# Kernel optimization log

Hardware: AMD Instinct MI355X
Metric: run time of the kernel (lower is better)

## Reference

```python
import jax, jax.numpy as jnp
import numpy as np

N_NODES = 100000
N_EDGES = 1600000
HIDDEN = 128
LEAKY_SLOPE = 0.01  # torch F.leaky_relu default


def setup_inputs() -> dict:
    key = jax.random.key(0)
    k1, k2, k3, k4 = jax.random.split(key, 4)
    x = jax.random.normal(k1, (N_NODES, HIDDEN), dtype=jnp.float32)
    edge_index = jax.random.randint(k2, (2, N_EDGES), 0, N_NODES, dtype=jnp.int64)
    # nn.Linear(hidden, 1, bias=False) weights, stored as [hidden] vectors
    w_i = jax.random.normal(k3, (HIDDEN,), dtype=jnp.float32) * (1.0 / np.sqrt(HIDDEN))
    w_j = jax.random.normal(k4, (HIDDEN,), dtype=jnp.float32) * (1.0 / np.sqrt(HIDDEN))
    return {"x": x, "edge_index": edge_index, "w_i": w_i, "w_j": w_j}


def _segment_softmax(e, seg, num_segments):
    # numerically stable softmax over variable-length groups keyed by seg
    seg_max = jax.ops.segment_max(e, seg, num_segments=num_segments)
    seg_max = jnp.where(jnp.isfinite(seg_max), seg_max, 0.0)  # empty segments
    e_exp = jnp.exp(e - seg_max[seg])
    denom = jax.ops.segment_sum(e_exp, seg, num_segments=num_segments)
    return e_exp / denom[seg]


def reference(x, edge_index, w_i, w_j):
    n = x.shape[0]
    idx_j = edge_index[0]  # edge_index_j (softmax groups)
    idx_i = edge_index[1]  # edge_index_i (aggregation destinations)
    # per-node attention logits, gathered per edge
    ei_all = x @ w_i  # [N]
    ej_all = x @ w_j  # [N]
    e = ei_all[idx_i] + ej_all[idx_j]  # [E]
    e = jnp.where(e > 0, e, LEAKY_SLOPE * e)  # leaky_relu
    alpha = _segment_softmax(e.astype(jnp.float32), idx_j, n)  # [E]
    # spmm(edge_index[[1,0]], alpha, N, N, x): out[idx_i] += alpha * x[idx_j]
    msgs = alpha[:, None] * x[idx_j]  # [E, hidden]
    out = jax.ops.segment_sum(msgs, idx_i, num_segments=n)
    return jax.nn.relu(out)
```

## Files before the change

### kernel.cpp

```cpp
#include <hip/hip_runtime.h>

#define N_HID 128
#define LEAKY 0.01f
#define EPB   2048
#define SCB   1024
#define TABV(g) (tab[g] + bs1[(g) >> 10])

__device__ inline int load_idx(const void* eidx, long long pos, int is64) {
    if (is64) return (int)((const long long*)eidx)[pos];
    return ((const int*)eidx)[pos];
}

__device__ inline int detect64(const void* eidx, int lane) {
    const long long* p = (const long long*)eidx;
    unsigned long long b = __ballot((p[lane] >> 32) != 0);
    return b == 0ull;
}

__global__ __launch_bounds__(256) void logits_hist_k(
        const float* __restrict__ x, const float* __restrict__ w_i,
        const float* __restrict__ w_j, float* __restrict__ ei_all,
        float* __restrict__ ej_all, signed char* __restrict__ xq,
        float* __restrict__ xs, const void* __restrict__ eidx,
        unsigned* __restrict__ tabI, unsigned* __restrict__ tabJ,
        int n, long long E, int nblkA, int NB) {
    __shared__ unsigned hi[512], hj[512];
    int lane = threadIdx.x & 63;
    if (blockIdx.x < (unsigned)nblkA) {
        for (int b = threadIdx.x; b < NB; b += 256) { hi[b] = 0; hj[b] = 0; }
        __syncthreads();
        int is64 = detect64(eidx, lane);
        long long k0 = (long long)blockIdx.x * EPB;
        #pragma unroll 4
        for (int m = 0; m < EPB / 256; ++m) {
            long long k = k0 + m * 256 + threadIdx.x;
            if (k < E) {
                int j = load_idx(eidx, k, is64);
                int i = load_idx(eidx, E + k, is64);
                atomicAdd(&hi[i >> 8], 1u);
                atomicAdd(&hj[j >> 8], 1u);
            }
        }
        __syncthreads();
        for (int b = threadIdx.x; b < NB; b += 256) {
            tabI[(size_t)b * nblkA + blockIdx.x] = hi[b];
            tabJ[(size_t)b * nblkA + blockIdx.x] = hj[b];
        }
    } else {
        int blk = blockIdx.x - nblkA;
        int wave = blk * 4 + (int)(threadIdx.x >> 6);
        if (wave >= n) return;
        const float2* xr = (const float2*)(x + (long long)wave * N_HID);
        float2 v  = xr[lane];
        float2 wi = ((const float2*)w_i)[lane];
        float2 wj = ((const float2*)w_j)[lane];
        float si = v.x * wi.x + v.y * wi.y;
        float sj = v.x * wj.x + v.y * wj.y;
        float am = fmaxf(fabsf(v.x), fabsf(v.y));
        #pragma unroll
        for (int off = 32; off >= 1; off >>= 1) {
            si += __shfl_xor(si, off);
            sj += __shfl_xor(sj, off);
            am = fmaxf(am, __shfl_xor(am, off));
        }
        if (xq) {
            float inv = 127.f / fmaxf(am, 1e-20f);
            int q0 = (int)rintf(v.x * inv);
            int q1 = (int)rintf(v.y * inv);
            q0 = min(127, max(-127, q0));
            q1 = min(127, max(-127, q1));
            ushort pk = (ushort)((q0 & 0xff) | ((q1 & 0xff) << 8));
            ((ushort*)(xq + (size_t)wave * N_HID))[lane] = pk;
        }
        if (lane == 0) {
            ei_all[wave] = si;
            ej_all[wave] = sj;
            if (xq) xs[wave] = fmaxf(am, 1e-20f) * (1.f / 127.f);
        }
    }
}

__global__ __launch_bounds__(SCB) void scanT1_k(unsigned* __restrict__ a,
                                                unsigned* __restrict__ bs, int nt) {
    __shared__ unsigned tmp[SCB];
    int gid = blockIdx.x * SCB + threadIdx.x;
    unsigned v = (gid < nt) ? a[gid] : 0;
    tmp[threadIdx.x] = v;
    __syncthreads();
    for (int off = 1; off < SCB; off <<= 1) {
        unsigned t = (threadIdx.x >= off) ? tmp[threadIdx.x - off] : 0;
        __syncthreads();
        tmp[threadIdx.x] += t;
        __syncthreads();
    }
    if (gid < nt) a[gid] = tmp[threadIdx.x] - v;
    if (threadIdx.x == SCB - 1) bs[blockIdx.x] = tmp[threadIdx.x];
}

__global__ __launch_bounds__(SCB) void scanT2_k(unsigned* __restrict__ bs, int nb) {
    __shared__ unsigned tmp[SCB];
    unsigned v = (threadIdx.x < nb) ? bs[threadIdx.x] : 0;
    tmp[threadIdx.x] = v;
    __syncthreads();
    for (int off = 1; off < SCB; off <<= 1) {
        unsigned t = (threadIdx.x >= off) ? tmp[threadIdx.x - off] : 0;
        __syncthreads();
        tmp[threadIdx.x] += t;
        __syncthreads();
    }
    if (threadIdx.x < nb) bs[threadIdx.x] = tmp[threadIdx.x] - v;
}

__global__ __launch_bounds__(256) void scatter2_k(
        const void* __restrict__ eidx, const unsigned* __restrict__ tab,
        const unsigned* __restrict__ bs1, unsigned* __restrict__ srecI,
        unsigned* __restrict__ srecJ, long long E, int nblkA, int NB, int NT) {
    __shared__ unsigned ci[512], cj[512];
    unsigned Eu = (unsigned)E;
    for (int b = threadIdx.x; b < NB; b += 256) {
        size_t gI = (size_t)b * nblkA + blockIdx.x;
        size_t gJ = (size_t)NT + gI;
        ci[b] = TABV(gI);
        cj[b] = TABV(gJ) - Eu;
    }
    __syncthreads();
    int is64 = detect64(eidx, threadIdx.x & 63);
    long long k0 = (long long)blockIdx.x * EPB;
    #pragma unroll 4
    for (int m = 0; m < EPB / 256; ++m) {
        long long k = k0 + m * 256 + threadIdx.x;
        if (k < E) {
            int j = load_idx(eidx, k, is64);
            int i = load_idx(eidx, E + k, is64);
            unsigned pI = atomicAdd(&ci[i >> 8], 1u);
            srecI[pI] = ((unsigned)(i & 255) << 17) | (unsigned)j;
            unsigned pJ = atomicAdd(&cj[j >> 8], 1u);
            srecJ[pJ] = ((unsigned)(j & 255) << 17) | (unsigned)i;
        }
    }
}

__global__ __launch_bounds__(512) void finalizeJ_k(
        const unsigned* __restrict__ srecJ, const unsigned* __restrict__ tab,
        const unsigned* __restrict__ bs1, const float* __restrict__ ei_all,
        const float* __restrict__ ej_all, float2* __restrict__ ejd,
        int n, long long E, int nblkA, int NB, int NT) {
    int b = blockIdx.x;
    int tid = threadIdx.x;
    unsigned Eu = (unsigned)E;
    size_t gJ0 = (size_t)NT + (size_t)b * nblkA;
    int base = (int)(TABV(gJ0) - Eu);
    int end  = (b + 1 < NB) ? (int)(TABV(gJ0 + nblkA) - Eu) : (int)E;

    __shared__ float ejl[256];
    __shared__ float dsum[256];
    int g = b * 256 + tid;
    if (tid < 256) {
        ejl[tid]  = (g < n) ? ej_all[g] : 0.f;
        dsum[tid] = 0.f;
    }
    __syncthreads();

    for (int t = base + tid; t < end; t += 512) {
        unsigned r = srecJ[t];
        int jl = (int)(r >> 17);
        int i  = (int)(r & 0x1FFFFu);
        float e = ei_all[i] + ejl[jl];
        e = e > 0.f ? e : LEAKY * e;
        atomicAdd(&dsum[jl], __expf(e));
    }
    __syncthreads();
    if (tid < 256 && g < n) {
        float2 r2;
        r2.x = ejl[tid];
        r2.y = dsum[tid];
        ejd[g] = r2;
    }
}

__global__ __launch_bounds__(512) void finalizeI_k(
        const unsigned* __restrict__ srecI, const unsigned* __restrict__ tab,
        const unsigned* __restrict__ bs1, const float* __restrict__ ei_all,
        const float2* __restrict__ ejd, int* __restrict__ start,
        unsigned* __restrict__ pje, int n, long long E, int nblkA, int NB,
        int NT) {
    int b = blockIdx.x;
    int tid = threadIdx.x;
    size_t gI0 = (size_t)b * nblkA;
    int base = (int)TABV(gI0);
    int end  = (b + 1 < NB) ? (int)TABV(gI0 + nblkA) : (int)E;

    __shared__ int cnt[256];
    __shared__ int off[256];
    __shared__ float eil[256];
    int g = b * 256 + tid;
    if (tid < 256) {
        cnt[tid] = 0;
        eil[tid] = (g < n) ? ei_all[g] : 0.f;
    }
    __syncthreads();

    for (int t = base + tid; t < end; t += 512)
        atomicAdd(&cnt[srecI[t] >> 17], 1);
    __syncthreads();

    int v = 0;
    if (tid < 256) { v = cnt[tid]; off[tid] = v; }
    __syncthreads();
    for (int s = 1; s < 256; s <<= 1) {
        int t2 = 0;
        if (tid < 256 && tid >= s) t2 = off[tid - s];
        __syncthreads();
        if (tid < 256) off[tid] += t2;
        __syncthreads();
    }
    if (tid < 256) {
        int excl = off[tid] - v;
        if (g < n) start[g] = base + excl;
        cnt[tid] = excl;
    }
    if (b == NB - 1 && tid == 0) start[n] = (int)E;
    __syncthreads();

    for (int t = base + tid; t < end; t += 512) {
        unsigned r = srecI[t];
        int il = (int)(r >> 17);
        int j  = (int)(r & 0x1FFFFu);
        float2 ed = ejd[j];
        float e = eil[il] + ed.x;
        e = e > 0.f ? e : LEAKY * e;
        float alpha = __expf(e) / ed.y;
        unsigned aq = __float2uint_rn(alpha * 32768.f);
        if (aq > 32767u) aq = 32767u;
        int slot = base + atomicAdd(&cnt[il], 1);
        pje[slot] = ((unsigned)j << 15) | aq;
    }
}

#define ACC4(w, A, B, C, D, af)                      \
    A += af * (float)((int)((w) << 24) >> 24);       \
    B += af * (float)((int)((w) << 16) >> 24);       \
    C += af * (float)((int)((w) <<  8) >> 24);       \
    D += af * (float)((int)(w) >> 24);

__global__ __launch_bounds__(256) void gather_i8_k(
        const int* __restrict__ start, const unsigned* __restrict__ pje,
        const signed char* __restrict__ xq, const float* __restrict__ xs,
        float* __restrict__ out, int n) {
    int wave = (int)((blockIdx.x * (long long)blockDim.x + threadIdx.x) >> 6);
    int lane = threadIdx.x & 63;
    if (wave >= n) return;
    int s = start[wave];
    int e_end = start[wave + 1];
    int sub = lane >> 3;
    int col = lane & 7;

    float t0 = 0.f, t1 = 0.f, t2 = 0.f, t3 = 0.f;
    float t4 = 0.f, t5 = 0.f, t6 = 0.f, t7 = 0.f;
    float t8 = 0.f, t9 = 0.f, tA = 0.f, tB = 0.f;
    float tC = 0.f, tD = 0.f, tE = 0.f, tF = 0.f;
    for (int e = s; e < e_end; e += 16) {
        int ee0 = e + sub;
        int ee1 = e + 8 + sub;
        unsigned c0 = (ee0 < e_end) ? pje[ee0] : 0u;
        unsigned c1 = (ee1 < e_end) ? pje[ee1] : 0u;
        int j0 = (int)(c0 >> 15), j1 = (int)(c1 >> 15);
        float a0 = (float)(c0 & 0x7FFFu) * (1.f / 32768.f) * xs[j0];
        float a1 = (float)(c1 & 0x7FFFu) * (1.f / 32768.f) * xs[j1];
        uint4 u0 = ((const uint4*)(xq + (size_t)j0 * N_HID))[col];
        uint4 u1 = ((const uint4*)(xq + (size_t)j1 * N_HID))[col];
        ACC4(u0.x, t0, t1, t2, t3, a0)
        ACC4(u0.y, t4, t5, t6, t7, a0)
        ACC4(u0.z, t8, t9, tA, tB, a0)
        ACC4(u0.w, tC, tD, tE, tF, a0)
        ACC4(u1.x, t0, t1, t2, t3, a1)
        ACC4(u1.y, t4, t5, t6, t7, a1)
        ACC4(u1.z, t8, t9, tA, tB, a1)
        ACC4(u1.w, tC, tD, tE, tF, a1)
    }
    #pragma unroll
    for (int off = 8; off <= 32; off <<= 1) {
        t0 += __shfl_xor(t0, off); t1 += __shfl_xor(t1, off);
        t2 += __shfl_xor(t2, off); t3 += __shfl_xor(t3, off);
        t4 += __shfl_xor(t4, off); t5 += __shfl_xor(t5, off);
        t6 += __shfl_xor(t6, off); t7 += __shfl_xor(t7, off);
        t8 += __shfl_xor(t8, off); t9 += __shfl_xor(t9, off);
        tA += __shfl_xor(tA, off); tB += __shfl_xor(tB, off);
        tC += __shfl_xor(tC, off); tD += __shfl_xor(tD, off);
        tE += __shfl_xor(tE, off); tF += __shfl_xor(tF, off);
    }
    if (sub == 0) {
        float4* orow = (float4*)(out + (size_t)wave * N_HID);
        float4 r;
        r.x = fmaxf(t0, 0.f); r.y = fmaxf(t1, 0.f);
        r.z = fmaxf(t2, 0.f); r.w = fmaxf(t3, 0.f);
        orow[col * 4 + 0] = r;
        r.x = fmaxf(t4, 0.f); r.y = fmaxf(t5, 0.f);
        r.z = fmaxf(t6, 0.f); r.w = fmaxf(t7, 0.f);
        orow[col * 4 + 1] = r;
        r.x = fmaxf(t8, 0.f); r.y = fmaxf(t9, 0.f);
        r.z = fmaxf(tA, 0.f); r.w = fmaxf(tB, 0.f);
        orow[col * 4 + 2] = r;
        r.x = fmaxf(tC, 0.f); r.y = fmaxf(tD, 0.f);
        r.z = fmaxf(tE, 0.f); r.w = fmaxf(tF, 0.f);
        orow[col * 4 + 3] = r;
    }
}

__global__ __launch_bounds__(256) void gather_f32_k(
        const int* __restrict__ start, const unsigned* __restrict__ pje,
        const float* __restrict__ x, float* __restrict__ out, int n) {
    int wave = (int)((blockIdx.x * (long long)blockDim.x + threadIdx.x) >> 6);
    int lane = threadIdx.x & 63;
    if (wave >= n) return;
    int s = start[wave];
    int e_end = start[wave + 1];
    float ax = 0.f, ay = 0.f;
    unsigned ja = 0;
    if (s < e_end) ja = pje[s];
    for (int e = s; e < e_end; ++e) {
        unsigned cur = ja;
        if (e + 1 < e_end) ja = pje[e + 1];
        float a = (float)(cur & 0x7FFFu) * (1.f / 32768.f);
        float2 v = ((const float2*)(x + (long long)(cur >> 15) * N_HID))[lane];
        ax += a * v.x;
        ay += a * v.y;
    }
    float2 r;
    r.x = fmaxf(ax, 0.f);
    r.y = fmaxf(ay, 0.f);
    ((float2*)(out + (long long)wave * N_HID))[lane] = r;
}

extern "C" void kernel_launch(void* const* d_in, const int* in_sizes, int n_in,
                              void* d_out, int out_size, void* d_ws,
                              size_t ws_size, hipStream_t stream) {
    const float* x   = (const float*)d_in[0];
    const void*  eix = d_in[1];
    const float* w_i = (const float*)d_in[2];
    const float* w_j = (const float*)d_in[3];
    float* out = (float*)d_out;

    int n = in_sizes[0] / N_HID;
    long long E = in_sizes[1] / 2;

    int nblkA = (int)((E + EPB - 1) / EPB);
    int nblkL = (n + 3) / 4;
    int NB    = (n + 255) / 256;
    int NT    = NB * nblkA;
    int NT2   = 2 * NT;
    int nb1   = (NT2 + SCB - 1) / SCB;

    char* p = (char*)d_ws;
    float* ei_all = (float*)p;               p += (size_t)n * 4;
    float* ej_all = (float*)p;               p += (size_t)n * 4;
    float2* ejd   = (float2*)p;              p += (size_t)n * 8;
    int*   start  = (int*)p;                 p += ((size_t)(n + 1) * 4 + 15) & ~15ull;
    unsigned* tab = (unsigned*)p;            p += ((size_t)NT2 * 4 + 15) & ~15ull;
    unsigned* tabI = tab;
    unsigned* tabJ = tab + NT;
    unsigned* bs1 = (unsigned*)p;            p += (size_t)SCB * 4;
    unsigned* srecI = (unsigned*)p;          p += (size_t)E * 4;
    unsigned* pje   = (unsigned*)p;          p += (size_t)E * 4;
    unsigned* srecJ = pje;
    signed char* xq = (signed char*)p;       p += ((size_t)n * N_HID + 15) & ~15ull;
    float* xs     = (float*)p;               p += (size_t)n * 4;
    int wsBig = ((size_t)(p - (char*)d_ws) <= ws_size);
    if (!wsBig) { xq = nullptr; xs = nullptr; }

    logits_hist_k<<<(unsigned)(nblkA + nblkL), 256, 0, stream>>>(
        x, w_i, w_j, ei_all, ej_all, xq, xs, eix, tabI, tabJ, n, E, nblkA, NB);

    scanT1_k<<<nb1, SCB, 0, stream>>>(tab, bs1, NT2);
    scanT2_k<<<1, SCB, 0, stream>>>(bs1, nb1);

    scatter2_k<<<nblkA, 256, 0, stream>>>(eix, tab, bs1, srecI, srecJ,
                                          E, nblkA, NB, NT);

    finalizeJ_k<<<NB, 512, 0, stream>>>(srecJ, tab, bs1, ei_all, ej_all, ejd,
                                        n, E, nblkA, NB, NT);

    finalizeI_k<<<NB, 512, 0, stream>>>(srecI, tab, bs1, ei_all, ejd,
                                        start, pje, n, E, nblkA, NB, NT);

    long long t4 = (long long)n * 64;
    if (wsBig) {
        gather_i8_k<<<(unsigned)((t4 + 255) / 256), 256, 0, stream>>>(
            start, pje, xq, xs, out, n);
    } else {
        gather_f32_k<<<(unsigned)((t4 + 255) / 256), 256, 0, stream>>>(
            start, pje, x, out, n);
    }
}
```

Baseline: 169.0 us.

## Fuse finalizeI and int8 gather into one block kernel with LDS edge list

Merges the per-destination alpha computation and the int8 gather-aggregate into one kernel. Each 1024-thread block buckets its 256 destination nodes' edges in shared memory (falling back to global when the block has more than CAP edges) and then aggregates them directly. This drops a kernel launch, the global pje write and read round trip, and the start array. finalizeJ is also moved to 1024 threads. The trade-off is fewer blocks (NB, about 391), each with 16 waves handling 16 nodes serially, which may lower gather parallelism and latency hiding.

```diff
diff --git a/kernel.cpp b/kernel.cpp
--- a/kernel.cpp
+++ b/kernel.cpp
@@ -4,6 +4,7 @@
 #define LEAKY 0.01f
 #define EPB   2048
 #define SCB   1024
+#define CAP   5120
 #define TABV(g) (tab[g] + bs1[(g) >> 10])
 
 __device__ inline int load_idx(const void* eidx, long long pos, int is64) {
@@ -140,7 +141,7 @@
     }
 }
 
-__global__ __launch_bounds__(512) void finalizeJ_k(
+__global__ __launch_bounds__(1024) void finalizeJ_k(
         const unsigned* __restrict__ srecJ, const unsigned* __restrict__ tab,
         const unsigned* __restrict__ bs1, const float* __restrict__ ei_all,
         const float* __restrict__ ej_all, float2* __restrict__ ejd,
@@ -161,7 +162,7 @@
     }
     __syncthreads();
 
-    for (int t = base + tid; t < end; t += 512) {
+    for (int t = base + tid; t < end; t += 1024) {
         unsigned r = srecJ[t];
         int jl = (int)(r >> 17);
         int i  = (int)(r & 0x1FFFFu);
@@ -175,6 +176,145 @@
         r2.x = ejl[tid];
         r2.y = dsum[tid];
         ejd[g] = r2;
+    }
+}
+
+#define ACC4(w, A, B, C, D, af)                      \
+    A += af * (float)((int)((w) << 24) >> 24);       \
+    B += af * (float)((int)((w) << 16) >> 24);       \
+    C += af * (float)((int)((w) <<  8) >> 24);       \
+    D += af * (float)((int)(w) >> 24);
+
+__global__ __launch_bounds__(1024) void finalizeI_gather_k(
+        const unsigned* __restrict__ srecI, const unsigned* __restrict__ tab,
+        const unsigned* __restrict__ bs1, const float* __restrict__ ei_all,
+        const float2* __restrict__ ejd, const signed char* __restrict__ xq,
+        const float* __restrict__ xs, unsigned* __restrict__ pjeG,
+        float* __restrict__ out, int n, long long E, int nblkA, int NB,
+        int NT) {
+    int b = blockIdx.x;
+    int tid = threadIdx.x;
+    size_t gI0 = (size_t)b * nblkA;
+    int base = (int)TABV(gI0);
+    int end  = (b + 1 < NB) ? (int)TABV(gI0 + nblkA) : (int)E;
+    bool useLds = (end - base) <= CAP;
+
+    __shared__ int cnt[256];
+    __shared__ int off[256];
+    __shared__ int lstart[256];
+    __shared__ float eil[256];
+    __shared__ unsigned pjeL[CAP];
+    int g = b * 256 + tid;
+    if (tid < 256) {
+        cnt[tid] = 0;
+        eil[tid] = (g < n) ? ei_all[g] : 0.f;
+    }
+    __syncthreads();
+
+    for (int t = base + tid; t < end; t += 1024)
+        atomicAdd(&cnt[srecI[t] >> 17], 1);
+    __syncthreads();
+
+    int v = 0;
+    if (tid < 256) { v = cnt[tid]; off[tid] = v; }
+    __syncthreads();
+    for (int s = 1; s < 256; s <<= 1) {
+        int t2 = 0;
+        if (tid < 256 && tid >= s) t2 = off[tid - s];
+        __syncthreads();
+        if (tid < 256) off[tid] += t2;
+        __syncthreads();
+    }
+    if (tid < 256) {
+        int excl = off[tid] - v;
+        lstart[tid] = excl;
+        cnt[tid] = excl;
+    }
+    __syncthreads();
+
+    for (int t = base + tid; t < end; t += 1024) {
+        unsigned r = srecI[t];
+        int il = (int)(r >> 17);
+        int j  = (int)(r & 0x1FFFFu);
+        float2 ed = ejd[j];
+        float e = eil[il] + ed.x;
+        e = e > 0.f ? e : LEAKY * e;
+        float alpha = __expf(e) / ed.y;
+        unsigned aq = __float2uint_rn(alpha * 32768.f);
+        if (aq > 32767u) aq = 32767u;
+        int slot = atomicAdd(&cnt[il], 1);
+        unsigned rec = ((unsigned)j << 15) | aq;
+        if (useLds) pjeL[slot] = rec;
+        else        pjeG[base + slot] = rec;
+    }
+    __syncthreads();
+
+    int wv   = tid >> 6;
+    int lane = tid & 63;
+    int sub  = lane >> 3;
+    int col  = lane & 7;
+    for (int nd = 0; nd < 16; ++nd) {
+        int il = wv * 16 + nd;
+        int gg = b * 256 + il;
+        if (gg >= n) break;
+        int s = lstart[il];
+        int e_end = cnt[il];
+        float t0 = 0.f, t1 = 0.f, t2 = 0.f, t3 = 0.f;
+        float t4 = 0.f, t5 = 0.f, t6 = 0.f, t7 = 0.f;
+        float t8 = 0.f, t9 = 0.f, tA = 0.f, tB = 0.f;
+        float tC = 0.f, tD = 0.f, tE = 0.f, tF = 0.f;
+        for (int e = s; e < e_end; e += 16) {
+            int ee0 = e + sub;
+            int ee1 = e + 8 + sub;
+            unsigned c0 = 0u, c1 = 0u;
+            if (useLds) {
+                if (ee0 < e_end) c0 = pjeL[ee0];
+                if (ee1 < e_end) c1 = pjeL[ee1];
+            } else {
+                if (ee0 < e_end) c0 = pjeG[base + ee0];
+                if (ee1 < e_end) c1 = pjeG[base + ee1];
+            }
+            int j0 = (int)(c0 >> 15), j1 = (int)(c1 >> 15);
+            float a0 = (float)(c0 & 0x7FFFu) * (1.f / 32768.f) * xs[j0];
+            float a1 = (float)(c1 & 0x7FFFu) * (1.f / 32768.f) * xs[j1];
+            uint4 u0 = ((const uint4*)(xq + (size_t)j0 * N_HID))[col];
+            uint4 u1 = ((const uint4*)(xq + (size_t)j1 * N_HID))[col];
+            ACC4(u0.x, t0, t1, t2, t3, a0)
+            ACC4(u0.y, t4, t5, t6, t7, a0)
+            ACC4(u0.z, t8, t9, tA, tB, a0)
+            ACC4(u0.w, tC, tD, tE, tF, a0)
+            ACC4(u1.x, t0, t1, t2, t3, a1)
+            ACC4(u1.y, t4, t5, t6, t7, a1)
+            ACC4(u1.z, t8, t9, tA, tB, a1)
+            ACC4(u1.w, tC, tD, tE, tF, a1)
+        }
+        #pragma unroll
+        for (int o = 8; o <= 32; o <<= 1) {
+            t0 += __shfl_xor(t0, o); t1 += __shfl_xor(t1, o);
+            t2 += __shfl_xor(t2, o); t3 += __shfl_xor(t3, o);
+            t4 += __shfl_xor(t4, o); t5 += __shfl_xor(t5, o);
+            t6 += __shfl_xor(t6, o); t7 += __shfl_xor(t7, o);
+            t8 += __shfl_xor(t8, o); t9 += __shfl_xor(t9, o);
+            tA += __shfl_xor(tA, o); tB += __shfl_xor(tB, o);
+            tC += __shfl_xor(tC, o); tD += __shfl_xor(tD, o);
+            tE += __shfl_xor(tE, o); tF += __shfl_xor(tF, o);
+        }
+        if (sub == 0) {
+            float4* orow = (float4*)(out + (size_t)gg * N_HID);
+            float4 r;
+            r.x = fmaxf(t0, 0.f); r.y = fmaxf(t1, 0.f);
+            r.z = fmaxf(t2, 0.f); r.w = fmaxf(t3, 0.f);
+            orow[col * 4 + 0] = r;
+            r.x = fmaxf(t4, 0.f); r.y = fmaxf(t5, 0.f);
+            r.z = fmaxf(t6, 0.f); r.w = fmaxf(t7, 0.f);
+            orow[col * 4 + 1] = r;
+            r.x = fmaxf(t8, 0.f); r.y = fmaxf(t9, 0.f);
+            r.z = fmaxf(tA, 0.f); r.w = fmaxf(tB, 0.f);
+            orow[col * 4 + 2] = r;
+            r.x = fmaxf(tC, 0.f); r.y = fmaxf(tD, 0.f);
+            r.z = fmaxf(tE, 0.f); r.w = fmaxf(tF, 0.f);
+            orow[col * 4 + 3] = r;
+        }
     }
 }
 
@@ -234,76 +374,6 @@
         if (aq > 32767u) aq = 32767u;
         int slot = base + atomicAdd(&cnt[il], 1);
         pje[slot] = ((unsigned)j << 15) | aq;
-    }
-}
-
-#define ACC4(w, A, B, C, D, af)                      \
-    A += af * (float)((int)((w) << 24) >> 24);       \
-    B += af * (float)((int)((w) << 16) >> 24);       \
-    C += af * (float)((int)((w) <<  8) >> 24);       \
-    D += af * (float)((int)(w) >> 24);
-
-__global__ __launch_bounds__(256) void gather_i8_k(
-        const int* __restrict__ start, const unsigned* __restrict__ pje,
-        const signed char* __restrict__ xq, const float* __restrict__ xs,
-        float* __restrict__ out, int n) {
-    int wave = (int)((blockIdx.x * (long long)blockDim.x + threadIdx.x) >> 6);
-    int lane = threadIdx.x & 63;
-    if (wave >= n) return;
-    int s = start[wave];
-    int e_end = start[wave + 1];
-    int sub = lane >> 3;
-    int col = lane & 7;
-
-    float t0 = 0.f, t1 = 0.f, t2 = 0.f, t3 = 0.f;
-    float t4 = 0.f, t5 = 0.f, t6 = 0.f, t7 = 0.f;
-    float t8 = 0.f, t9 = 0.f, tA = 0.f, tB = 0.f;
-    float tC = 0.f, tD = 0.f, tE = 0.f, tF = 0.f;
-    for (int e = s; e < e_end; e += 16) {
-        int ee0 = e + sub;
-        int ee1 = e + 8 + sub;
-        unsigned c0 = (ee0 < e_end) ? pje[ee0] : 0u;
-        unsigned c1 = (ee1 < e_end) ? pje[ee1] : 0u;
-        int j0 = (int)(c0 >> 15), j1 = (int)(c1 >> 15);
-        float a0 = (float)(c0 & 0x7FFFu) * (1.f / 32768.f) * xs[j0];
-        float a1 = (float)(c1 & 0x7FFFu) * (1.f / 32768.f) * xs[j1];
-        uint4 u0 = ((const uint4*)(xq + (size_t)j0 * N_HID))[col];
-        uint4 u1 = ((const uint4*)(xq + (size_t)j1 * N_HID))[col];
-        ACC4(u0.x, t0, t1, t2, t3, a0)
-        ACC4(u0.y, t4, t5, t6, t7, a0)
-        ACC4(u0.z, t8, t9, tA, tB, a0)
-        ACC4(u0.w, tC, tD, tE, tF, a0)
-        ACC4(u1.x, t0, t1, t2, t3, a1)
-        ACC4(u1.y, t4, t5, t6, t7, a1)
-        ACC4(u1.z, t8, t9, tA, tB, a1)
-        ACC4(u1.w, tC, tD, tE, tF, a1)
-    }
-    #pragma unroll
-    for (int off = 8; off <= 32; off <<= 1) {
-        t0 += __shfl_xor(t0, off); t1 += __shfl_xor(t1, off);
-        t2 += __shfl_xor(t2, off); t3 += __shfl_xor(t3, off);
-        t4 += __shfl_xor(t4, off); t5 += __shfl_xor(t5, off);
-        t6 += __shfl_xor(t6, off); t7 += __shfl_xor(t7, off);
-        t8 += __shfl_xor(t8, off); t9 += __shfl_xor(t9, off);
-        tA += __shfl_xor(tA, off); tB += __shfl_xor(tB, off);
-        tC += __shfl_xor(tC, off); tD += __shfl_xor(tD, off);
-        tE += __shfl_xor(tE, off); tF += __shfl_xor(tF, off);
-    }
-    if (sub == 0) {
-        float4* orow = (float4*)(out + (size_t)wave * N_HID);
-        float4 r;
-        r.x = fmaxf(t0, 0.f); r.y = fmaxf(t1, 0.f);
-        r.z = fmaxf(t2, 0.f); r.w = fmaxf(t3, 0.f);
-        orow[col * 4 + 0] = r;
-        r.x = fmaxf(t4, 0.f); r.y = fmaxf(t5, 0.f);
-        r.z = fmaxf(t6, 0.f); r.w = fmaxf(t7, 0.f);
-        orow[col * 4 + 1] = r;
-        r.x = fmaxf(t8, 0.f); r.y = fmaxf(t9, 0.f);
-        r.z = fmaxf(tA, 0.f); r.w = fmaxf(tB, 0.f);
-        orow[col * 4 + 2] = r;
-        r.x = fmaxf(tC, 0.f); r.y = fmaxf(tD, 0.f);
-        r.z = fmaxf(tE, 0.f); r.w = fmaxf(tF, 0.f);
-        orow[col * 4 + 3] = r;
     }
 }
 
@@ -377,17 +447,16 @@
     scatter2_k<<<nblkA, 256, 0, stream>>>(eix, tab, bs1, srecI, srecJ,
                                           E, nblkA, NB, NT);
 
-    finalizeJ_k<<<NB, 512, 0, stream>>>(srecJ, tab, bs1, ei_all, ej_all, ejd,
-                                        n, E, nblkA, NB, NT);
-
-    finalizeI_k<<<NB, 512, 0, stream>>>(srecI, tab, bs1, ei_all, ejd,
-                                        start, pje, n, E, nblkA, NB, NT);
-
-    long long t4 = (long long)n * 64;
+    finalizeJ_k<<<NB, 1024, 0, stream>>>(srecJ, tab, bs1, ei_all, ej_all, ejd,
+                                         n, E, nblkA, NB, NT);
+
     if (wsBig) {
-        gather_i8_k<<<(unsigned)((t4 + 255) / 256), 256, 0, stream>>>(
-            start, pje, xq, xs, out, n);
+        finalizeI_gather_k<<<NB, 1024, 0, stream>>>(
+            srecI, tab, bs1, ei_all, ejd, xq, xs, pje, out, n, E, nblkA, NB, NT);
     } else {
+        finalizeI_k<<<NB, 512, 0, stream>>>(srecI, tab, bs1, ei_all, ejd,
+                                            start, pje, n, E, nblkA, NB, NT);
+        long long t4 = (long long)n * 64;
         gather_f32_k<<<(unsigned)((t4 + 255) / 256), 256, 0, stream>>>(
             start, pje, x, out, n);
     }
```

Result: slower. 183.4 us (+8.5%).
